# Kernel optimization log

Hardware: AMD Instinct MI355X
Metric: run time of the kernel (lower is better)

The kernel has to match this reference:

```python
import jax, jax.numpy as jnp
import numpy as np

N = 100000
E = 1600000
D_IN = 128
D_OUT = 128


def setup_inputs() -> dict:
    key = jax.random.key(0)
    k1, k2, k3, k4 = jax.random.split(key, 4)
    x = jax.random.normal(k1, (N, D_IN), dtype=jnp.float32)
    edge_index = jax.random.randint(k2, (2, E), 0, N, dtype=jnp.int64)
    # GCNConv params: glorot weight, zero bias
    scale = jnp.sqrt(6.0 / (D_IN + D_OUT)).astype(jnp.float32)
    W = jax.random.uniform(k3, (D_IN, D_OUT), dtype=jnp.float32, minval=-scale, maxval=scale)
    b = jnp.zeros((D_OUT,), dtype=jnp.float32)
    return {"x": x, "edge_index": edge_index, "W": W, "b": b}


def reference(x, edge_index, W, b):
    n = x.shape[0]
    # add self-loops (PyG GCNConv default: add_self_loops=True)
    loops = jnp.arange(n, dtype=edge_index.dtype)
    src = jnp.concatenate([edge_index[0], loops])
    dst = jnp.concatenate([edge_index[1], loops])
    # symmetric normalization: deg computed at target nodes
    ones = jnp.ones_like(dst, dtype=x.dtype)
    deg = jax.ops.segment_sum(ones, dst, num_segments=n)
    dinv = jnp.where(deg > 0, jax.lax.rsqrt(deg), 0.0)
    norm = dinv[src] * dinv[dst]  # [E+N]
    # linear transform then gather-scale-scatter aggregation
    h = x @ W  # [N, D_OUT]
    msgs = h[src] * norm[:, None]  # [E+N, D_OUT]
    out = jax.ops.segment_sum(msgs, dst, num_segments=n)
    return out + b
```

## Files before the change

kernel.cpp:

```cpp
#include <hip/hip_runtime.h>

#define D 128
#define CAP 5120

typedef __attribute__((ext_vector_type(4))) float f32x4;
typedef __attribute__((ext_vector_type(8))) short s16x8;

static __device__ __forceinline__ ushort f2bf(float f) {
    unsigned u = __float_as_uint(f);
    u += 0x7fffu + ((u >> 16) & 1u);
    return (ushort)(u >> 16);
}
static __device__ __forceinline__ float bf_lo(unsigned u) {
    return __uint_as_float(u << 16);
}
static __device__ __forceinline__ float bf_hi(unsigned u) {
    return __uint_as_float(u & 0xFFFF0000u);
}

__global__ __launch_bounds__(256) void k_wt(const float* __restrict__ W,
                                            ushort* __restrict__ WT,
                                            int* __restrict__ gcursor) {
    int i = blockIdx.x * 256 + threadIdx.x;
    if (blockIdx.x < 2) gcursor[blockIdx.x * 256 + threadIdx.x] = 0;
    int nn = i >> 7, k = i & 127;
    WT[i] = f2bf(W[k * D + nn]);
}

__global__ __launch_bounds__(1024) void k_part(const int* __restrict__ src,
                                               const int* __restrict__ dst,
                                               int e, int nbins,
                                               int* __restrict__ gcursor,
                                               unsigned* __restrict__ praw) {
    __shared__ int hist[512];
    int tid = threadIdx.x;
    for (int j = tid; j < nbins; j += 1024) hist[j] = 0;
    __syncthreads();

    int chunk = (e + gridDim.x - 1) / gridDim.x;
    int lo = blockIdx.x * chunk;
    int hi = lo + chunk; if (hi > e) hi = e;

    for (int i = lo + tid; i < hi; i += 1024)
        atomicAdd(&hist[dst[i] >> 8], 1);
    __syncthreads();

    for (int j = tid; j < nbins; j += 1024)
        hist[j] = atomicAdd(&gcursor[j], hist[j]);
    __syncthreads();

    for (int i = lo + tid; i < hi; i += 1024) {
        int d = dst[i];
        int bin = d >> 8;
        int pos = atomicAdd(&hist[bin], 1);
        if (pos < CAP)
            praw[(size_t)bin * CAP + pos] = ((unsigned)(d & 255) << 24) | (unsigned)src[i];
    }
}

__global__ __launch_bounds__(1024) void k_fine(unsigned* __restrict__ praw,
                                               const int* __restrict__ gcursor,
                                               int n,
                                               int* __restrict__ deg,
                                               float* __restrict__ dinv,
                                               int* __restrict__ offs) {
    __shared__ int hist[256], scanv[256], cur[256];
    __shared__ unsigned stage[CAP];
    int b = blockIdx.x, tid = threadIdx.x;
    int base = b * CAP;
    int cnt = gcursor[b]; if (cnt > CAP) cnt = CAP;

    if (tid < 256) hist[tid] = 0;
    __syncthreads();
    for (int i = tid; i < cnt; i += 1024)
        atomicAdd(&hist[praw[base + i] >> 24], 1);
    __syncthreads();

    if (tid < 256) scanv[tid] = hist[tid];
    __syncthreads();
    for (int off = 1; off < 256; off <<= 1) {
        int t = 0;
        if (tid < 256 && tid >= off) t = scanv[tid - off];
        __syncthreads();
        if (tid < 256) scanv[tid] += t;
        __syncthreads();
    }
    if (tid < 256) {
        int ex = scanv[tid] - hist[tid];
        cur[tid] = ex;
        int d0 = b * 256 + tid;
        if (d0 < n) {
            deg[d0]  = hist[tid];
            dinv[d0] = rsqrtf((float)hist[tid] + 1.f);
            offs[d0] = base + ex;
        }
    }
    __syncthreads();

    for (int i = tid; i < cnt; i += 1024) {
        unsigned p = praw[base + i];
        int pos = atomicAdd(&cur[p >> 24], 1);
        stage[pos] = p & 0xFFFFFFu;
    }
    __syncthreads();
    for (int i = tid; i < cnt; i += 1024)
        praw[base + i] = stage[i];
}

__global__ __launch_bounds__(256, 2) void k_gemm_mfma(const float* __restrict__ x,
                                                      const ushort* __restrict__ WT,
                                                      const float* __restrict__ dinv,
                                                      ushort* __restrict__ h,
                                                      int n, int nchunks) {
    int lane = threadIdx.x & 63;
    int wid  = threadIdx.x >> 6;
    int lr = lane & 15;
    int lk = lane >> 4;

    s16x8 bfrag[8][4];
#pragma unroll
    for (int nt = 0; nt < 8; ++nt)
#pragma unroll
        for (int kk = 0; kk < 4; ++kk)
            bfrag[nt][kk] = *reinterpret_cast<const s16x8*>(
                WT + (nt * 16 + lr) * D + kk * 32 + lk * 8);

    int stride = gridDim.x * 4;
    for (int chunk = blockIdx.x * 4 + wid; chunk < nchunks; chunk += stride) {
        int r0 = chunk * 16;
        int ar = r0 + lr;
        if (ar > n - 1) ar = n - 1;

        s16x8 afrag[4];
#pragma unroll
        for (int kk = 0; kk < 4; ++kk) {
            const float4* p = reinterpret_cast<const float4*>(x) +
                              (size_t)ar * 32 + kk * 8 + lk * 2;
            float4 u = p[0];
            float4 v = p[1];
            s16x8 a;
            a[0] = (short)f2bf(u.x); a[1] = (short)f2bf(u.y);
            a[2] = (short)f2bf(u.z); a[3] = (short)f2bf(u.w);
            a[4] = (short)f2bf(v.x); a[5] = (short)f2bf(v.y);
            a[6] = (short)f2bf(v.z); a[7] = (short)f2bf(v.w);
            afrag[kk] = a;
        }

        f32x4 acc[8];
#pragma unroll
        for (int nt = 0; nt < 8; ++nt) acc[nt] = (f32x4){0.f, 0.f, 0.f, 0.f};

#pragma unroll
        for (int kk = 0; kk < 4; ++kk)
#pragma unroll
            for (int nt = 0; nt < 8; ++nt)
                acc[nt] = __builtin_amdgcn_mfma_f32_16x16x32_bf16(
                    afrag[kk], bfrag[nt][kk], acc[nt], 0, 0, 0);

#pragma unroll
        for (int i = 0; i < 4; ++i) {
            int row = r0 + lk * 4 + i;
            if (row < n) {
                float di = dinv[row];
#pragma unroll
                for (int nt = 0; nt < 8; ++nt)
                    h[(size_t)row * D + nt * 16 + lr] = f2bf(acc[nt][i] * di);
            }
        }
    }
}

__global__ __launch_bounds__(256) void k_gather(const unsigned* __restrict__ pairs,
                                                const int* __restrict__ offs,
                                                const int* __restrict__ deg,
                                                const float* __restrict__ dinv,
                                                const ushort* __restrict__ h,
                                                const float* __restrict__ b,
                                                float* __restrict__ out, int n) {
    int g = (blockIdx.x * 256 + threadIdx.x) >> 4;
    if (g >= n) return;
    int lane = threadIdx.x & 15;
    const uint4* h16 = reinterpret_cast<const uint4*>(h);

    float a0, a1, a2, a3, a4, a5, a6, a7;
    {
        uint4 v = h16[(size_t)g * 16 + lane];
        a0 = bf_lo(v.x); a1 = bf_hi(v.x);
        a2 = bf_lo(v.y); a3 = bf_hi(v.y);
        a4 = bf_lo(v.z); a5 = bf_hi(v.z);
        a6 = bf_lo(v.w); a7 = bf_hi(v.w);
    }

    int st  = offs[g];
    int cnt = deg[g];
    int k = 0;
    for (; k + 7 < cnt; k += 8) {
        uint4 v[8];
#pragma unroll
        for (int j = 0; j < 8; ++j) {
            int s0 = (int)pairs[st + k + j];
            v[j] = h16[(size_t)s0 * 16 + lane];
        }
#pragma unroll
        for (int j = 0; j < 8; ++j) {
            a0 += bf_lo(v[j].x); a1 += bf_hi(v[j].x);
            a2 += bf_lo(v[j].y); a3 += bf_hi(v[j].y);
            a4 += bf_lo(v[j].z); a5 += bf_hi(v[j].z);
            a6 += bf_lo(v[j].w); a7 += bf_hi(v[j].w);
        }
    }
    if (k + 3 < cnt) {
        uint4 v[4];
#pragma unroll
        for (int j = 0; j < 4; ++j) {
            int s0 = (int)pairs[st + k + j];
            v[j] = h16[(size_t)s0 * 16 + lane];
        }
#pragma unroll
        for (int j = 0; j < 4; ++j) {
            a0 += bf_lo(v[j].x); a1 += bf_hi(v[j].x);
            a2 += bf_lo(v[j].y); a3 += bf_hi(v[j].y);
            a4 += bf_lo(v[j].z); a5 += bf_hi(v[j].z);
            a6 += bf_lo(v[j].w); a7 += bf_hi(v[j].w);
        }
        k += 4;
    }
    for (; k < cnt; ++k) {
        int s0 = (int)pairs[st + k];
        uint4 v0 = h16[(size_t)s0 * 16 + lane];
        a0 += bf_lo(v0.x); a1 += bf_hi(v0.x);
        a2 += bf_lo(v0.y); a3 += bf_hi(v0.y);
        a4 += bf_lo(v0.z); a5 += bf_hi(v0.z);
        a6 += bf_lo(v0.w); a7 += bf_hi(v0.w);
    }

    float dd = dinv[g];
    const float4* b4 = reinterpret_cast<const float4*>(b);
    float4 blo = b4[lane * 2], bhi = b4[lane * 2 + 1];
    float4 olo, ohi;
    olo.x = a0 * dd + blo.x; olo.y = a1 * dd + blo.y;
    olo.z = a2 * dd + blo.z; olo.w = a3 * dd + blo.w;
    ohi.x = a4 * dd + bhi.x; ohi.y = a5 * dd + bhi.y;
    ohi.z = a6 * dd + bhi.z; ohi.w = a7 * dd + bhi.w;
    float4* o4 = reinterpret_cast<float4*>(out + (size_t)g * D + lane * 8);
    o4[0] = olo;
    o4[1] = ohi;
}

extern "C" void kernel_launch(void* const* d_in, const int* in_sizes, int n_in,
                              void* d_out, int out_size, void* d_ws, size_t ws_size,
                              hipStream_t stream) {
    const float* x  = (const float*)d_in[0];
    const int*   ei = (const int*)d_in[1];
    const float* W  = (const float*)d_in[2];
    const float* b  = (const float*)d_in[3];
    float* out = (float*)d_out;

    int n = in_sizes[0] / D;
    int e = in_sizes[1] / 2;
    const int* src = ei;
    const int* dst = ei + e;
    int nbins = (n + 255) >> 8;

    char* ws = (char*)d_ws;
    ushort*   h       = (ushort*)ws;    ws += (size_t)n * D * 2;
    ushort*   WT      = (ushort*)ws;    ws += (size_t)D * D * 2;
    int*      deg     = (int*)ws;       ws += (size_t)n * 4;
    float*    dinv    = (float*)ws;     ws += (size_t)n * 4;
    int*      offs    = (int*)ws;       ws += (size_t)n * 4;
    int*      gcursor = (int*)ws;       ws += 512 * 4;
    unsigned* praw    = (unsigned*)ws;

    k_wt<<<64, 256, 0, stream>>>(W, WT, gcursor);

    k_part<<<128, 1024, 0, stream>>>(src, dst, e, nbins, gcursor, praw);

    k_fine<<<nbins, 1024, 0, stream>>>(praw, gcursor, n, deg, dinv, offs);

    int nchunks = (n + 15) / 16;
    k_gemm_mfma<<<512, 256, 0, stream>>>(x, WT, dinv, h, n, nchunks);

    int nb = (n * 16 + 255) / 256;
    k_gather<<<nb, 256, 0, stream>>>(praw, offs, deg, dinv, h, b, out, n);
}
```

Baseline: 122.6 us.

## Stage MFMA-fragment-ordered weights in LDS and launch one chunk per wave

The transposed bf16 weight is now written in MFMA B-fragment order, so each block can copy it into LDS with coalesced loads and each wave reads fragments from LDS instead of keeping all 32 in registers. Register pressure drops, so launch bounds raise occupancy to 4 blocks per SM. The persistent grid-stride loop is replaced by one 16-row chunk per wave, with a grid sized to the chunk count. The partition kernel grid is also doubled. Each block pays a 32KB LDS fill and a barrier, and each MFMA now waits on an LDS read.

```diff
diff --git a/kernel.cpp b/kernel.cpp
--- a/kernel.cpp
+++ b/kernel.cpp
@@ -19,12 +19,18 @@
 }
 
 __global__ __launch_bounds__(256) void k_wt(const float* __restrict__ W,
-                                            ushort* __restrict__ WT,
+                                            ushort* __restrict__ WTf,
                                             int* __restrict__ gcursor) {
     int i = blockIdx.x * 256 + threadIdx.x;
     if (blockIdx.x < 2) gcursor[blockIdx.x * 256 + threadIdx.x] = 0;
-    int nn = i >> 7, k = i & 127;
-    WT[i] = f2bf(W[k * D + nn]);
+    int j    = i & 7;
+    int lane = (i >> 3) & 63;
+    int frag = i >> 9;
+    int kk   = frag & 3;
+    int nt   = frag >> 2;
+    int nn = nt * 16 + (lane & 15);
+    int k  = kk * 32 + (lane >> 4) * 8 + j;
+    WTf[i] = f2bf(W[k * D + nn]);
 }
 
 __global__ __launch_bounds__(1024) void k_part(const int* __restrict__ src,
@@ -107,65 +113,68 @@
         praw[base + i] = stage[i];
 }
 
-__global__ __launch_bounds__(256, 2) void k_gemm_mfma(const float* __restrict__ x,
-                                                      const ushort* __restrict__ WT,
+__global__ __launch_bounds__(256, 4) void k_gemm_mfma(const float* __restrict__ x,
+                                                      const ushort* __restrict__ WTf,
                                                       const float* __restrict__ dinv,
                                                       ushort* __restrict__ h,
                                                       int n, int nchunks) {
+    __shared__ uint4 wlds[2048];
+
+    {
+        const uint4* g = reinterpret_cast<const uint4*>(WTf);
+#pragma unroll
+        for (int t = 0; t < 8; ++t)
+            wlds[t * 256 + threadIdx.x] = g[t * 256 + threadIdx.x];
+    }
+    __syncthreads();
+
     int lane = threadIdx.x & 63;
     int wid  = threadIdx.x >> 6;
     int lr = lane & 15;
     int lk = lane >> 4;
 
-    s16x8 bfrag[8][4];
-#pragma unroll
-    for (int nt = 0; nt < 8; ++nt)
-#pragma unroll
-        for (int kk = 0; kk < 4; ++kk)
-            bfrag[nt][kk] = *reinterpret_cast<const s16x8*>(
-                WT + (nt * 16 + lr) * D + kk * 32 + lk * 8);
-
-    int stride = gridDim.x * 4;
-    for (int chunk = blockIdx.x * 4 + wid; chunk < nchunks; chunk += stride) {
-        int r0 = chunk * 16;
-        int ar = r0 + lr;
-        if (ar > n - 1) ar = n - 1;
-
-        s16x8 afrag[4];
-#pragma unroll
-        for (int kk = 0; kk < 4; ++kk) {
-            const float4* p = reinterpret_cast<const float4*>(x) +
-                              (size_t)ar * 32 + kk * 8 + lk * 2;
-            float4 u = p[0];
-            float4 v = p[1];
-            s16x8 a;
-            a[0] = (short)f2bf(u.x); a[1] = (short)f2bf(u.y);
-            a[2] = (short)f2bf(u.z); a[3] = (short)f2bf(u.w);
-            a[4] = (short)f2bf(v.x); a[5] = (short)f2bf(v.y);
-            a[6] = (short)f2bf(v.z); a[7] = (short)f2bf(v.w);
-            afrag[kk] = a;
-        }
-
-        f32x4 acc[8];
-#pragma unroll
-        for (int nt = 0; nt < 8; ++nt) acc[nt] = (f32x4){0.f, 0.f, 0.f, 0.f};
-
-#pragma unroll
-        for (int kk = 0; kk < 4; ++kk)
+    int chunk = blockIdx.x * 4 + wid;
+    if (chunk >= nchunks) return;
+    int r0 = chunk * 16;
+    int ar = r0 + lr; if (ar > n - 1) ar = n - 1;
+
+    s16x8 afrag[4];
+#pragma unroll
+    for (int kk = 0; kk < 4; ++kk) {
+        const float4* p = reinterpret_cast<const float4*>(x) +
+                          (size_t)ar * 32 + kk * 8 + lk * 2;
+        float4 u = p[0];
+        float4 v = p[1];
+        s16x8 a;
+        a[0] = (short)f2bf(u.x); a[1] = (short)f2bf(u.y);
+        a[2] = (short)f2bf(u.z); a[3] = (short)f2bf(u.w);
+        a[4] = (short)f2bf(v.x); a[5] = (short)f2bf(v.y);
+        a[6] = (short)f2bf(v.z); a[7] = (short)f2bf(v.w);
+        afrag[kk] = a;
+    }
+
+    f32x4 acc[8];
+#pragma unroll
+    for (int nt = 0; nt < 8; ++nt) acc[nt] = (f32x4){0.f, 0.f, 0.f, 0.f};
+
+    const s16x8* wl = reinterpret_cast<const s16x8*>(wlds);
+#pragma unroll
+    for (int kk = 0; kk < 4; ++kk)
+#pragma unroll
+        for (int nt = 0; nt < 8; ++nt) {
+            s16x8 bfrag = wl[(nt * 4 + kk) * 64 + lane];
+            acc[nt] = __builtin_amdgcn_mfma_f32_16x16x32_bf16(
+                afrag[kk], bfrag, acc[nt], 0, 0, 0);
+        }
+
+#pragma unroll
+    for (int i = 0; i < 4; ++i) {
+        int row = r0 + lk * 4 + i;
+        if (row < n) {
+            float di = dinv[row];
 #pragma unroll
             for (int nt = 0; nt < 8; ++nt)
-                acc[nt] = __builtin_amdgcn_mfma_f32_16x16x32_bf16(
-                    afrag[kk], bfrag[nt][kk], acc[nt], 0, 0, 0);
-
-#pragma unroll
-        for (int i = 0; i < 4; ++i) {
-            int row = r0 + lk * 4 + i;
-            if (row < n) {
-                float di = dinv[row];
-#pragma unroll
-                for (int nt = 0; nt < 8; ++nt)
-                    h[(size_t)row * D + nt * 16 + lr] = f2bf(acc[nt][i] * di);
-            }
+                h[(size_t)row * D + nt * 16 + lr] = f2bf(acc[nt][i] * di);
         }
     }
 }
@@ -264,21 +273,21 @@
 
     char* ws = (char*)d_ws;
     ushort*   h       = (ushort*)ws;    ws += (size_t)n * D * 2;
-    ushort*   WT      = (ushort*)ws;    ws += (size_t)D * D * 2;
+    ushort*   WTf     = (ushort*)ws;    ws += (size_t)D * D * 2;
     int*      deg     = (int*)ws;       ws += (size_t)n * 4;
     float*    dinv    = (float*)ws;     ws += (size_t)n * 4;
     int*      offs    = (int*)ws;       ws += (size_t)n * 4;
     int*      gcursor = (int*)ws;       ws += 512 * 4;
     unsigned* praw    = (unsigned*)ws;
 
-    k_wt<<<64, 256, 0, stream>>>(W, WT, gcursor);
-
-    k_part<<<128, 1024, 0, stream>>>(src, dst, e, nbins, gcursor, praw);
+    k_wt<<<64, 256, 0, stream>>>(W, WTf, gcursor);
+
+    k_part<<<256, 1024, 0, stream>>>(src, dst, e, nbins, gcursor, praw);
 
     k_fine<<<nbins, 1024, 0, stream>>>(praw, gcursor, n, deg, dinv, offs);
 
     int nchunks = (n + 15) / 16;
-    k_gemm_mfma<<<512, 256, 0, stream>>>(x, WT, dinv, h, n, nchunks);
+    k_gemm_mfma<<<(nchunks + 3) / 4, 256, 0, stream>>>(x, WTf, dinv, h, n, nchunks);
 
     int nb = (n * 16 + 255) / 256;
     k_gather<<<nb, 256, 0, stream>>>(praw, offs, deg, dinv, h, b, out, n);
```

Result: faster. 114.0 us (-7.0%).
